# Kernel tuning notes

Hardware: AMD Instinct MI355X
Metric: run time of the kernel (lower is better)

## Reference

```python
import jax, jax.numpy as jnp
import numpy as np

TEMPERATURE = 0.1
NSAMPLE = 32
B, N_PER, M_PER, C_FEAT = 2, 16384, 4096, 64


def setup_inputs() -> dict:
    key = jax.random.key(0)
    ks = jax.random.split(key, 4)
    xyz = jax.random.normal(ks[0], (B * N_PER, 3), jnp.float32)
    new_xyz = jax.random.normal(ks[1], (B * M_PER, 3), jnp.float32)
    new_xyz_r = jax.random.uniform(ks[2], (B * M_PER, 1), jnp.float32, minval=0.5, maxval=1.0)
    features = jax.random.normal(ks[3], (B * N_PER, C_FEAT), jnp.float32)
    xyz_batch_cnt = jnp.full((B,), N_PER, jnp.int32)
    new_xyz_batch_cnt = jnp.full((B,), M_PER, jnp.int32)
    temperature_decay = jnp.ones((1,), jnp.float32)
    return dict(xyz=xyz, xyz_batch_cnt=xyz_batch_cnt, new_xyz=new_xyz,
                new_xyz_r=new_xyz_r, new_xyz_batch_cnt=new_xyz_batch_cnt,
                features=features, temperature_decay=temperature_decay)


def _ball_query(xyz_b, new_xyz_b, r_b, nsample):
    # xyz_b: (B,N,3), new_xyz_b: (B,M,3), r_b: (B,M)
    # Returns idx (B,M,nsample) int32 (batch-local point indices, first-in-order
    # within the ball, remaining slots filled with first hit, 0 if empty) and
    # empty mask (B,M) bool. Mirrors the CUDA ball_query_deform kernel.
    N = xyz_b.shape[1]
    d2 = jnp.sum((new_xyz_b[:, :, None, :] - xyz_b[:, None, :, :]) ** 2, axis=-1)  # (B,M,N)
    within = d2 < (r_b ** 2)[..., None]
    # key = point index if within radius else N; top_k of -key gives the first
    # nsample in-ball indices in ascending index order.
    key = jnp.where(within, jnp.arange(N, dtype=jnp.int32), jnp.int32(N))
    neg_vals, _ = jax.lax.top_k(-key, nsample)
    cand = -neg_vals  # (B,M,nsample)
    cnt = within.sum(axis=-1)  # (B,M)
    slot_valid = jnp.arange(nsample) < cnt[..., None]
    idx = jnp.where(slot_valid, cand, cand[..., :1])  # pad with first found index
    empty = cnt == 0
    idx = jnp.where(empty[..., None], 0, idx)
    return idx.astype(jnp.int32), empty


def reference(xyz, xyz_batch_cnt, new_xyz, new_xyz_r, new_xyz_batch_cnt, features, temperature_decay):
    b = xyz_batch_cnt.shape[0]
    n = xyz.shape[0] // b
    m = new_xyz.shape[0] // b
    c = features.shape[1]
    real_t = TEMPERATURE * temperature_decay[0]
    explore_r = new_xyz_r + real_t * 5.0  # (M_tot, 1)

    xyz_b = xyz.reshape(b, n, 3)
    nxyz_b = new_xyz.reshape(b, m, 3)
    idx_b, empty_b = _ball_query(xyz_b, nxyz_b, explore_r.reshape(b, m), NSAMPLE)

    gather = jax.vmap(lambda pts, i: pts[i])  # per-batch gather

    grouped_xyz = gather(xyz_b, idx_b)                 # (B,M,ns,3)
    grouped_xyz = grouped_xyz - nxyz_b[:, :, None, :]  # center
    grouped_xyz = jnp.where(empty_b[:, :, None, None], 0.0, grouped_xyz)
    grouped_xyz = grouped_xyz.reshape(b * m, NSAMPLE, 3).transpose(0, 2, 1)  # (M_tot,3,ns)

    dist_xyz = jnp.sqrt(jnp.sum(grouped_xyz * grouped_xyz, axis=1))  # (M_tot,ns)
    weights = 1.0 - jax.nn.sigmoid((dist_xyz - new_xyz_r) / real_t)  # (M_tot,ns)

    feat_b = features.reshape(b, n, c)
    grouped_feat = gather(feat_b, idx_b)  # (B,M,ns,C)
    grouped_feat = jnp.where(empty_b[:, :, None, None], 0.0, grouped_feat)
    grouped_feat = grouped_feat.reshape(b * m, NSAMPLE, c).transpose(0, 2, 1)  # (M_tot,C,ns)

    new_features = jnp.concatenate([grouped_xyz, grouped_feat], axis=1)  # (M_tot,3+C,ns)
    idx = idx_b.reshape(b * m, NSAMPLE)
    return new_features, weights, idx
```

## Files before the change

kernel.cpp:

```cpp
#include <hip/hip_runtime.h>
#include <math.h>

#define NS 32
#define WPB 4

__global__ __launch_bounds__(256) void qgd_kernel(
    const float* __restrict__ xyz,
    const float* __restrict__ new_xyz,
    const float* __restrict__ new_xyz_r,
    const float* __restrict__ features,
    const float* __restrict__ tdec,
    float* __restrict__ out,
    int N_per, int M_per, int C, int M_tot)
{
#pragma clang fp contract(off)

    __shared__ int sIdx[WPB][NS];

    const int lane = threadIdx.x & 63;
    const int wv   = threadIdx.x >> 6;
    const int m    = blockIdx.x * WPB + wv;
    const bool active = (m < M_tot);

    int   cnt = 0;
    float qx = 0.f, qy = 0.f, qz = 0.f, r_orig = 0.f, real_t = 0.1f;
    const float* xb = xyz;
    int b = 0;

    if (active) {
        b  = m / M_per;
        qx = new_xyz[(size_t)m * 3 + 0];
        qy = new_xyz[(size_t)m * 3 + 1];
        qz = new_xyz[(size_t)m * 3 + 2];
        r_orig = new_xyz_r[m];
        real_t = 0.1f * tdec[0];
        float er  = r_orig + real_t * 5.0f;
        float er2 = er * er;
        xb = xyz + (size_t)b * N_per * 3;

        const unsigned long long lt = (1ull << lane) - 1ull;

        int base = 0;
        for (; base + 256 <= N_per; base += 256) {
            float d2k[4];
            #pragma unroll
            for (int k = 0; k < 4; ++k) {
                const float* pp = xb + (size_t)(base + k * 64 + lane) * 3;
                float dx = pp[0] - qx;
                float dy = pp[1] - qy;
                float dz = pp[2] - qz;
                float d2 = dx * dx;
                d2 = d2 + dy * dy;
                d2 = d2 + dz * dz;
                d2k[k] = d2;
            }
            #pragma unroll
            for (int k = 0; k < 4; ++k) {
                bool hit = d2k[k] < er2;
                unsigned long long msk = __ballot(hit);
                if (hit) {
                    int slot = cnt + (int)__popcll(msk & lt);
                    if (slot < NS) sIdx[wv][slot] = base + k * 64 + lane;
                }
                cnt += (int)__popcll(msk);
            }
            if (cnt >= NS) break;
        }
        if (cnt < NS) {
            for (; base < N_per; base += 64) {
                int p = base + lane;
                bool inb = p < N_per;
                int pc = inb ? p : (N_per - 1);
                const float* pp = xb + (size_t)pc * 3;
                float dx = pp[0] - qx;
                float dy = pp[1] - qy;
                float dz = pp[2] - qz;
                float d2 = dx * dx;
                d2 = d2 + dy * dy;
                d2 = d2 + dz * dz;
                bool hit = inb && (d2 < er2);
                unsigned long long msk = __ballot(hit);
                if (hit) {
                    int slot = cnt + (int)__popcll(msk & lt);
                    if (slot < NS) sIdx[wv][slot] = p;
                }
                cnt += (int)__popcll(msk);
                if (cnt >= NS) break;
            }
        }
    }
    __syncthreads();

    const bool empty = (cnt == 0);
    if (active && lane < NS && lane >= cnt) {
        sIdx[wv][lane] = empty ? 0 : sIdx[wv][0];
    }
    __syncthreads();

    if (!active) return;

    const int    j       = lane & 31;
    const int    h       = lane >> 5;
    const int    pj      = sIdx[wv][j];
    const size_t nf_base = (size_t)m * (3 + C) * NS;
    float* wout = out + (size_t)M_tot * (3 + C) * NS;
    float* iout = wout + (size_t)M_tot * NS;

    if (lane < NS) {
        float gx = 0.f, gy = 0.f, gz = 0.f;
        if (!empty) {
            gx = xb[(size_t)pj * 3 + 0] - qx;
            gy = xb[(size_t)pj * 3 + 1] - qy;
            gz = xb[(size_t)pj * 3 + 2] - qz;
        }
        float d2 = gx * gx;
        d2 = d2 + gy * gy;
        d2 = d2 + gz * gz;
        float dist = sqrtf(d2);
        float wt = 1.0f / (1.0f + expf((dist - r_orig) / real_t));
        out[nf_base + 0 * NS + j] = gx;
        out[nf_base + 1 * NS + j] = gy;
        out[nf_base + 2 * NS + j] = gz;
        wout[(size_t)m * NS + j] = wt;
        iout[(size_t)m * NS + j] = (float)pj;
    }

    const float* frow = features + ((size_t)b * N_per + pj) * C;
    for (int t = 0; t < C; t += 8) {
        float4 v = make_float4(0.f, 0.f, 0.f, 0.f);
        if (!empty) v = *(const float4*)(frow + t + h * 4);
        const size_t cb = nf_base + (size_t)(3 + t + h * 4) * NS + j;
        out[cb + 0 * NS] = v.x;
        out[cb + 1 * NS] = v.y;
        out[cb + 2 * NS] = v.z;
        out[cb + 3 * NS] = v.w;
    }
}

extern "C" void kernel_launch(void* const* d_in, const int* in_sizes, int n_in,
                              void* d_out, int out_size, void* d_ws, size_t ws_size,
                              hipStream_t stream) {
    const float* xyz       = (const float*)d_in[0];
    const float* new_xyz   = (const float*)d_in[2];
    const float* new_xyz_r = (const float*)d_in[3];
    const float* features  = (const float*)d_in[5];
    const float* tdec      = (const float*)d_in[6];

    const int B     = in_sizes[1];
    const int N_tot = in_sizes[0] / 3;
    const int M_tot = in_sizes[2] / 3;
    const int C     = in_sizes[5] / N_tot;
    const int N_per = N_tot / B;
    const int M_per = M_tot / B;

    const int blocks = (M_tot + WPB - 1) / WPB;
    qgd_kernel<<<blocks, 256, 0, stream>>>(xyz, new_xyz, new_xyz_r, features,
                                           tdec, (float*)d_out,
                                           N_per, M_per, C, M_tot);
}
```

Baseline: 139.1 us.

## Split ball query into prefix scan, straggler scan, and transposed feature write

The single fused kernel becomes three kernels. The first scans only the first 2048 points per query and pushes unfinished queries onto a worklist through an atomic counter. The second gives each straggler a whole block, splitting the point range across four waves and merging their hits in order. The third gathers features and transposes them through shared memory so global stores are coalesced float4 writes. This targets load imbalance from queries with few neighbours and the strided output stores, at the cost of extra launches, a memset, and an index round trip through the output buffer.

```diff
diff --git a/kernel.cpp b/kernel.cpp
--- a/kernel.cpp
+++ b/kernel.cpp
@@ -3,56 +3,110 @@
 
 #define NS 32
 #define WPB 4
-
-__global__ __launch_bounds__(256) void qgd_kernel(
-    const float* __restrict__ xyz,
-    const float* __restrict__ new_xyz,
-    const float* __restrict__ new_xyz_r,
-    const float* __restrict__ features,
-    const float* __restrict__ tdec,
-    float* __restrict__ out,
-    int N_per, int M_per, int C, int M_tot)
+#define SCAN0 2048
+#define TSTRIDE 36
+
+__global__ __launch_bounds__(256) void qgd_scanA(
+    const float* __restrict__ xyz, const float* __restrict__ new_xyz,
+    const float* __restrict__ new_xyz_r, const float* __restrict__ tdec,
+    int* __restrict__ idx_out,
+    int* __restrict__ counter, int* __restrict__ list,
+    int N_per, int M_per, int M_tot)
 {
 #pragma clang fp contract(off)
-
-    __shared__ int sIdx[WPB][NS];
-
     const int lane = threadIdx.x & 63;
     const int wv   = threadIdx.x >> 6;
     const int m    = blockIdx.x * WPB + wv;
-    const bool active = (m < M_tot);
-
-    int   cnt = 0;
-    float qx = 0.f, qy = 0.f, qz = 0.f, r_orig = 0.f, real_t = 0.1f;
-    const float* xb = xyz;
-    int b = 0;
-
-    if (active) {
-        b  = m / M_per;
-        qx = new_xyz[(size_t)m * 3 + 0];
-        qy = new_xyz[(size_t)m * 3 + 1];
-        qz = new_xyz[(size_t)m * 3 + 2];
-        r_orig = new_xyz_r[m];
-        real_t = 0.1f * tdec[0];
-        float er  = r_orig + real_t * 5.0f;
-        float er2 = er * er;
-        xb = xyz + (size_t)b * N_per * 3;
-
-        const unsigned long long lt = (1ull << lane) - 1ull;
-
-        int base = 0;
-        for (; base + 256 <= N_per; base += 256) {
+    if (m >= M_tot) return;
+
+    const int bb = m / M_per;
+    const float* xb = xyz + (size_t)bb * N_per * 3;
+    const float qx = new_xyz[(size_t)m * 3 + 0];
+    const float qy = new_xyz[(size_t)m * 3 + 1];
+    const float qz = new_xyz[(size_t)m * 3 + 2];
+    const float r_orig = new_xyz_r[m];
+    const float real_t = 0.1f * tdec[0];
+    const float er  = r_orig + real_t * 5.0f;
+    const float er2 = er * er;
+    const unsigned long long lt = (1ull << lane) - 1ull;
+
+    const int scan0 = (SCAN0 < N_per) ? SCAN0 : N_per;
+    int cnt = 0;
+    for (int base = 0; base < scan0; base += 256) {
+        float d2k[4];
+        #pragma unroll
+        for (int k = 0; k < 4; ++k) {
+            int p = base + k * 64 + lane;
+            int pc = (p < N_per) ? p : (N_per - 1);
+            const float* pp = xb + (size_t)pc * 3;
+            float dx = pp[0] - qx, dy = pp[1] - qy, dz = pp[2] - qz;
+            float d2 = dx * dx;
+            d2 = d2 + dy * dy;
+            d2 = d2 + dz * dz;
+            d2k[k] = (p < N_per) ? d2 : 1e30f;
+        }
+        #pragma unroll
+        for (int k = 0; k < 4; ++k) {
+            bool hit = d2k[k] < er2;
+            unsigned long long msk = __ballot(hit);
+            if (hit) {
+                int slot = cnt + (int)__popcll(msk & lt);
+                if (slot < NS) idx_out[(size_t)m * NS + slot] = base + k * 64 + lane;
+            }
+            cnt += (int)__popcll(msk);
+        }
+        if (cnt >= NS) break;
+    }
+    if (cnt < NS && lane == 0) {
+        int pos = atomicAdd(counter, 1);
+        list[pos] = m;
+    }
+}
+
+__global__ __launch_bounds__(256) void qgd_scanB(
+    const float* __restrict__ xyz, const float* __restrict__ new_xyz,
+    const float* __restrict__ new_xyz_r, const float* __restrict__ tdec,
+    int* __restrict__ idx_out,
+    const int* __restrict__ counter, const int* __restrict__ list,
+    int N_per, int M_per)
+{
+#pragma clang fp contract(off)
+    __shared__ int sH[WPB][NS];
+    __shared__ int sC[WPB];
+
+    const int lane = threadIdx.x & 63;
+    const int wv   = threadIdx.x >> 6;
+    const int nstrag = *counter;
+    const unsigned long long lt = (1ull << lane) - 1ull;
+
+    for (int it = blockIdx.x; it < nstrag; it += gridDim.x) {
+        const int m  = list[it];
+        const int bb = m / M_per;
+        const float* xb = xyz + (size_t)bb * N_per * 3;
+        const float qx = new_xyz[(size_t)m * 3 + 0];
+        const float qy = new_xyz[(size_t)m * 3 + 1];
+        const float qz = new_xyz[(size_t)m * 3 + 2];
+        const float r_orig = new_xyz_r[m];
+        const float real_t = 0.1f * tdec[0];
+        const float er  = r_orig + real_t * 5.0f;
+        const float er2 = er * er;
+
+        const int rb = (int)(((long long)N_per * wv) / WPB);
+        const int re = (int)(((long long)N_per * (wv + 1)) / WPB);
+
+        int cnt = 0;
+        for (int base = rb; base < re; base += 256) {
             float d2k[4];
             #pragma unroll
             for (int k = 0; k < 4; ++k) {
-                const float* pp = xb + (size_t)(base + k * 64 + lane) * 3;
-                float dx = pp[0] - qx;
-                float dy = pp[1] - qy;
-                float dz = pp[2] - qz;
+                int p = base + k * 64 + lane;
+                int pc = (p < re) ? p : (re - 1);
+                const float* pp = xb + (size_t)pc * 3;
+                float dx = pp[0] - qx, dy = pp[1] - qy, dz = pp[2] - qz;
                 float d2 = dx * dx;
                 d2 = d2 + dy * dy;
                 d2 = d2 + dz * dz;
-                d2k[k] = d2;
+                d2k[k] = (p < re) ? d2 : 1e30f;
             }
             #pragma unroll
             for (int k = 0; k < 4; ++k) {
@@ -60,53 +114,79 @@
                 unsigned long long msk = __ballot(hit);
                 if (hit) {
                     int slot = cnt + (int)__popcll(msk & lt);
-                    if (slot < NS) sIdx[wv][slot] = base + k * 64 + lane;
+                    if (slot < NS) sH[wv][slot] = base + k * 64 + lane;
                 }
                 cnt += (int)__popcll(msk);
             }
             if (cnt >= NS) break;
         }
-        if (cnt < NS) {
-            for (; base < N_per; base += 64) {
-                int p = base + lane;
-                bool inb = p < N_per;
-                int pc = inb ? p : (N_per - 1);
-                const float* pp = xb + (size_t)pc * 3;
-                float dx = pp[0] - qx;
-                float dy = pp[1] - qy;
-                float dz = pp[2] - qz;
-                float d2 = dx * dx;
-                d2 = d2 + dy * dy;
-                d2 = d2 + dz * dz;
-                bool hit = inb && (d2 < er2);
-                unsigned long long msk = __ballot(hit);
-                if (hit) {
-                    int slot = cnt + (int)__popcll(msk & lt);
-                    if (slot < NS) sIdx[wv][slot] = p;
-                }
-                cnt += (int)__popcll(msk);
-                if (cnt >= NS) break;
-            }
-        }
-    }
-    __syncthreads();
-
-    const bool empty = (cnt == 0);
-    if (active && lane < NS && lane >= cnt) {
-        sIdx[wv][lane] = empty ? 0 : sIdx[wv][0];
-    }
-    __syncthreads();
-
-    if (!active) return;
-
-    const int    j       = lane & 31;
-    const int    h       = lane >> 5;
-    const int    pj      = sIdx[wv][j];
-    const size_t nf_base = (size_t)m * (3 + C) * NS;
+        if (lane == 0) sC[wv] = (cnt < NS) ? cnt : NS;
+        __syncthreads();
+
+        if (threadIdx.x < NS) {
+            const int j  = threadIdx.x;
+            const int c0 = sC[0], c1 = sC[1], c2 = sC[2], c3 = sC[3];
+            const int o1 = c0, o2 = c0 + c1, o3 = o2 + c2;
+            const int tot = o3 + c3;
+            int v = 0;
+            if (j < tot) {
+                if      (j >= o3) v = sH[3][j - o3];
+                else if (j >= o2) v = sH[2][j - o2];
+                else if (j >= o1) v = sH[1][j - o1];
+                else              v = sH[0][j];
+            }
+            int first = -1;
+            if      (c0 > 0) first = sH[0][0];
+            else if (c1 > 0) first = sH[1][0];
+            else if (c2 > 0) first = sH[2][0];
+            else if (c3 > 0) first = sH[3][0];
+            int outv;
+            if (tot == 0)      outv = (j == 0) ? -1 : 0;
+            else if (j < tot)  outv = v;
+            else               outv = first;
+            idx_out[(size_t)m * NS + j] = outv;
+        }
+        __syncthreads();
+    }
+}
+
+__global__ __launch_bounds__(256) void qgd_writeC(
+    const float* __restrict__ xyz, const float* __restrict__ new_xyz,
+    const float* __restrict__ new_xyz_r, const float* __restrict__ features,
+    const float* __restrict__ tdec, float* __restrict__ out,
+    int N_per, int M_per, int C, int M_tot)
+{
+#pragma clang fp contract(off)
+    __shared__ __align__(16) float sBuf[WPB * 32 * TSTRIDE];
+    __shared__ int sIdx[WPB][NS];
+
+    const int lane = threadIdx.x & 63;
+    const int wv   = threadIdx.x >> 6;
+    const int m    = blockIdx.x * WPB + wv;
+    const bool active = (m < M_tot);
+
     float* wout = out + (size_t)M_tot * (3 + C) * NS;
     float* iout = wout + (size_t)M_tot * NS;
+    int*   iint = (int*)iout;
+
+    if (active && lane < NS) sIdx[wv][lane] = iint[(size_t)m * NS + lane];
+    __syncthreads();
+
+    if (!active) return;
+
+    const bool empty = (sIdx[wv][0] < 0);
+    const int  bb    = m / M_per;
+    const float* xb  = xyz + (size_t)bb * N_per * 3;
+    const int    j   = lane & 31;
+    const size_t nf_base = (size_t)m * (3 + C) * NS;
 
     if (lane < NS) {
+        const float qx = new_xyz[(size_t)m * 3 + 0];
+        const float qy = new_xyz[(size_t)m * 3 + 1];
+        const float qz = new_xyz[(size_t)m * 3 + 2];
+        const float r_orig = new_xyz_r[m];
+        const float real_t = 0.1f * tdec[0];
+        const int pj = empty ? 0 : sIdx[wv][j];
         float gx = 0.f, gy = 0.f, gz = 0.f;
         if (!empty) {
             gx = xb[(size_t)pj * 3 + 0] - qx;
@@ -125,15 +205,48 @@
         iout[(size_t)m * NS + j] = (float)pj;
     }
 
-    const float* frow = features + ((size_t)b * N_per + pj) * C;
-    for (int t = 0; t < C; t += 8) {
-        float4 v = make_float4(0.f, 0.f, 0.f, 0.f);
-        if (!empty) v = *(const float4*)(frow + t + h * 4);
-        const size_t cb = nf_base + (size_t)(3 + t + h * 4) * NS + j;
-        out[cb + 0 * NS] = v.x;
-        out[cb + 1 * NS] = v.y;
-        out[cb + 2 * NS] = v.z;
-        out[cb + 3 * NS] = v.w;
+    float* sT = sBuf + wv * (32 * TSTRIDE);
+    const float* fb = features + (size_t)bb * N_per * C;
+
+    int c0 = 0;
+    for (; c0 + 32 <= C; c0 += 32) {
+        {
+            const int k  = lane & 7;
+            const int f4 = 4 * (k & 3);
+            #pragma unroll
+            for (int t = 0; t < 4; ++t) {
+                const int r  = 8 * t + (lane >> 3);
+                const int pj = empty ? 0 : sIdx[wv][r];
+                float4 v = make_float4(0.f, 0.f, 0.f, 0.f);
+                if (!empty) v = *(const float4*)(fb + (size_t)pj * C + c0 + 4 * k);
+                const int rs = r ^ f4;
+                sT[(4 * k + 0) * TSTRIDE + rs] = v.x;
+                sT[(4 * k + 1) * TSTRIDE + rs] = v.y;
+                sT[(4 * k + 2) * TSTRIDE + rs] = v.z;
+                sT[(4 * k + 3) * TSTRIDE + rs] = v.w;
+            }
+        }
+        __syncthreads();
+        {
+            const int jg = lane & 7;
+            #pragma unroll
+            for (int s2 = 0; s2 < 4; ++s2) {
+                const int ch = 8 * s2 + (lane >> 3);
+                const int jb = (4 * jg) ^ (4 * ((ch >> 2) & 3));
+                float4 w = *(const float4*)&sT[ch * TSTRIDE + jb];
+                *(float4*)&out[nf_base + (size_t)(3 + c0 + ch) * NS + 4 * jg] = w;
+            }
+        }
+        __syncthreads();
+    }
+    if (c0 < C) {
+        const int h  = lane >> 5;
+        const int pj = empty ? 0 : sIdx[wv][j];
+        const float* frow = fb + (size_t)pj * C;
+        for (int c = c0 + h; c < C; c += 2) {
+            float v = empty ? 0.f : frow[c];
+            out[nf_base + (size_t)(3 + c) * NS + j] = v;
+        }
     }
 }
 
@@ -153,8 +266,20 @@
     const int N_per = N_tot / B;
     const int M_per = M_tot / B;
 
-    const int blocks = (M_tot + WPB - 1) / WPB;
-    qgd_kernel<<<blocks, 256, 0, stream>>>(xyz, new_xyz, new_xyz_r, features,
-                                           tdec, (float*)d_out,
-                                           N_per, M_per, C, M_tot);
-}
+    float* out  = (float*)d_out;
+    int*   iint = (int*)(out + (size_t)M_tot * (3 + C) * NS + (size_t)M_tot * NS);
+    int*   counter = (int*)d_ws;
+    int*   list    = (int*)d_ws + 4;
+
+    hipMemsetAsync(counter, 0, sizeof(int), stream);
+
+    const int blocksA = (M_tot + WPB - 1) / WPB;
+    qgd_scanA<<<blocksA, 256, 0, stream>>>(xyz, new_xyz, new_xyz_r, tdec,
+                                           iint, counter, list,
+                                           N_per, M_per, M_tot);
+    qgd_scanB<<<512, 256, 0, stream>>>(xyz, new_xyz, new_xyz_r, tdec,
+                                       iint, counter, list, N_per, M_per);
+    const int blocksC = (M_tot + WPB - 1) / WPB;
+    qgd_writeC<<<blocksC, 256, 0, stream>>>(xyz, new_xyz, new_xyz_r, features,
+                                            tdec, out, N_per, M_per, C, M_tot);
+}
```

Result: faster. 124.2 us (-10.7%).
